# Optimization experiments

Hardware: AMD Instinct MI355X
Metric: run time of the kernel (lower is better)

Reference implementation:

```python
import jax, jax.numpy as jnp
import numpy as np

N_NODES = 100000
N_EDGES = 1600000
STATE_DIM = 128
HIDDEN_DIM = 128
ACTION_DIM = 16


def gcn_conv(x, edge_index, W, b, n_nodes):
    """PyG-style GCNConv: add self-loops, symmetric normalization, x@W then aggregate."""
    xw = x @ W  # [N, H]
    loops = jnp.arange(n_nodes, dtype=edge_index.dtype)
    src = jnp.concatenate([edge_index[0], loops])  # [E+N]
    dst = jnp.concatenate([edge_index[1], loops])
    ones = jnp.ones(src.shape[0], dtype=xw.dtype)
    deg = jax.ops.segment_sum(ones, dst, num_segments=n_nodes)  # degree of target nodes
    dinv = jnp.where(deg > 0, jax.lax.rsqrt(deg), 0.0)
    norm = dinv[src] * dinv[dst]  # [E+N]
    msg = xw[src] * norm[:, None]  # gather + scale (irregular access)
    out = jax.ops.segment_sum(msg, dst, num_segments=n_nodes)  # scatter-aggregate
    return out + b


def setup_inputs() -> dict:
    key = jax.random.key(0)
    ks = jax.random.split(key, 12)
    def lin(k, fan_in, shape):
        bound = 1.0 / np.sqrt(fan_in)
        return jax.random.uniform(k, shape, jnp.float32, -bound, bound)
    return {
        "x": jax.random.normal(ks[0], (N_NODES, STATE_DIM), jnp.float32),
        "edge_index": jax.random.randint(ks[1], (2, N_EDGES), 0, N_NODES, jnp.int64),
        "action": jax.random.normal(ks[2], (N_NODES, ACTION_DIM), jnp.float32),
        "gcn1_w": lin(ks[3], STATE_DIM, (STATE_DIM, HIDDEN_DIM)),
        "gcn1_b": lin(ks[4], STATE_DIM, (HIDDEN_DIM,)),
        "gcn2_w": lin(ks[5], HIDDEN_DIM, (HIDDEN_DIM, HIDDEN_DIM)),
        "gcn2_b": lin(ks[6], HIDDEN_DIM, (HIDDEN_DIM,)),
        "fc1_w": lin(ks[7], HIDDEN_DIM + ACTION_DIM, (HIDDEN_DIM + ACTION_DIM, HIDDEN_DIM)),
        "fc1_b": lin(ks[8], HIDDEN_DIM + ACTION_DIM, (HIDDEN_DIM,)),
        "fc2_w": lin(ks[9], HIDDEN_DIM, (HIDDEN_DIM, 1)),
        "fc2_b": lin(ks[10], HIDDEN_DIM, (1,)),
    }


def reference(x, edge_index, action, gcn1_w, gcn1_b, gcn2_w, gcn2_b, fc1_w, fc1_b, fc2_w, fc2_b):
    n = x.shape[0]
    h = jax.nn.relu(gcn_conv(x, edge_index, gcn1_w, gcn1_b, n))
    h = jax.nn.relu(gcn_conv(h, edge_index, gcn2_w, gcn2_b, n))
    h = jnp.concatenate([h, action], axis=-1)  # [N, H+A]
    h = jax.nn.relu(h @ fc1_w + fc1_b)
    q = h @ fc2_w + fc2_b  # [N, 1]
    return q.squeeze(-1)
```

## Files before the change

kernel.cpp:

```cpp
#include <hip/hip_runtime.h>
#include <hip/hip_bf16.h>

typedef unsigned short u16;
typedef unsigned int   u32;
typedef __attribute__((ext_vector_type(8))) short bf16x8;
typedef __attribute__((ext_vector_type(4))) float f32x4;

constexpr int NN = 100000;
constexpr int NE = 1600000;
constexpr int D  = 128;
constexpr size_t WS_NEED = 58909184;

constexpr int NBUCK = 196;
constexpr int NBLKA = 256;
constexpr int EPB   = 6272;
constexpr int CAPA  = 80;

__device__ __forceinline__ float bf2f(u16 u){ union{u32 i;float f;}v; v.i=((u32)u)<<16; return v.f; }
__device__ __forceinline__ float2 bfp(u32 u){ union{u32 i;float f;}a,b; a.i=u<<16; b.i=u&0xffff0000u; return make_float2(a.f,b.f); }
__device__ __forceinline__ u16 f2bf(float f){ union{float f;u32 i;}v; v.f=f; u32 r=v.i + 0x7fffu + ((v.i>>16)&1u); return (u16)(r>>16); }
__device__ __forceinline__ u32 pk2(float a, float b){ return (u32)f2bf(a) | ((u32)f2bf(b)<<16); }

__global__ void detect_kernel(const u32* __restrict__ xw, const int* __restrict__ ei,
                              int* __restrict__ flagf, int* __restrict__ flage){
  __shared__ int shf[256];
  __shared__ int she[256];
  int t = threadIdx.x;
  int cnt = 0;
  for(int i = 0; i < 16; i++){
    u32 w = xw[(t*16 + i) * 256];
    int e = (int)((w >> 7) & 0xFFu);
    cnt += (e >= 64 && e <= 160) ? 1 : 0;
  }
  int nz = 0;
  for(int i = 0; i < 8; i++){
    int k = t*8 + i;
    long long w = 1 + ((long long)k * (2LL*NE - 2)) / 2048;
    nz += (ei[(int)(w | 1)] != 0) ? 1 : 0;
  }
  shf[t] = cnt; she[t] = nz;
  __syncthreads();
  for(int off=128; off>0; off>>=1){
    if(t<off){ shf[t]+=shf[t+off]; she[t]+=she[t+off]; }
    __syncthreads();
  }
  if(t==0){ flagf[0] = (shf[0] < 3000) ? 1 : 0; flage[0] = (she[0] == 0) ? 1 : 0; }
}

__global__ void prep_kernel(const void* __restrict__ w1, const void* __restrict__ w2,
    const void* __restrict__ fw1, const void* __restrict__ b1, const void* __restrict__ b2,
    const void* __restrict__ fb1, const void* __restrict__ fw2, const void* __restrict__ fb2,
    const int* __restrict__ flagf,
    u16* __restrict__ WT1, u16* __restrict__ WT2, u16* __restrict__ WTF, float* __restrict__ BF)
{
  const int ff = flagf[0];
  int i = blockIdx.x*256 + threadIdx.x;
  auto cv = [&](const void* p, int idx)->float{
    return ff ? ((const float*)p)[idx] : bf2f(((const u16*)p)[idx]);
  };
  if(i < 16384){
    int k = i >> 7, d = i & 127;
    WT1[d*128 + k] = f2bf(cv(w1, i));
  }else if(i < 32768){
    int j = i - 16384; int k = j >> 7, d = j & 127;
    WT2[d*128 + k] = f2bf(cv(w2, j));
  }else if(i < 51200){
    int j = i - 32768; int k = j >> 7, d = j & 127;
    WTF[d*144 + k] = f2bf(cv(fw1, j));
  }else if(i < 51713){
    int j = i - 51200;
    if(j < 128)       BF[j]   = cv(b1, j);
    else if(j < 256)  BF[j]   = cv(b2, j-128);
    else if(j < 384)  BF[j]   = cv(fb1, j-256);
    else if(j < 512)  BF[j]   = cv(fw2, j-384);
    else              BF[512] = cv(fb2, 0);
  }
}

__global__ void fill1_kernel(u16* __restrict__ out, int n){
  int i = blockIdx.x*blockDim.x + threadIdx.x;
  if(i < n) out[i] = 0x3F80;
}

__global__ __launch_bounds__(256) void passA_kernel(
    const int* __restrict__ ei, const int* __restrict__ flage,
    u32* __restrict__ ebuf, u32* __restrict__ counts)
{
  __shared__ u32 hist[NBUCK];
  int t = threadIdx.x;
  for(int b = t; b < NBUCK; b += 256) hist[b] = 0;
  __syncthreads();
  const int f = flage[0];
  const int eb = blockIdx.x * EPB;
  const u32 cbase = blockIdx.x * NBUCK;
  for(int i = t; i < EPB; i += 256){
    int e = eb + i;
    if(e >= NE) break;
    int s = f ? ei[2*e]      : ei[e];
    int d = f ? ei[2*(NE+e)] : ei[NE+e];
    if((u32)s >= (u32)NN || (u32)d >= (u32)NN) continue;
    int b = d >> 9;
    u32 rank = atomicAdd(&hist[b], 1u);
    if(rank < CAPA) ebuf[(size_t)(cbase + b)*CAPA + rank] = (u32)s | ((u32)(d & 511) << 17);
  }
  __syncthreads();
  for(int b = t; b < NBUCK; b += 256){
    u32 c = hist[b];
    counts[cbase + b] = (c < CAPA) ? c : CAPA;
  }
}

__global__ void scan196_kernel(const u32* __restrict__ counts, int* __restrict__ bases){
  __shared__ int sh[NBUCK];
  int t = threadIdx.x;
  if(t < NBUCK){
    int tot = 0;
    for(int c = 0; c < NBLKA; c++) tot += counts[c*NBUCK + t];
    sh[t] = tot;
  }
  __syncthreads();
  if(t == 0){
    int acc = 0;
    for(int b = 0; b < NBUCK; b++){ int v = sh[b]; sh[b] = acc; acc += v; }
  }
  __syncthreads();
  if(t < NBUCK) bases[t] = sh[t];
}

__global__ __launch_bounds__(512) void passB_kernel(
    const u32* __restrict__ ebuf, const u32* __restrict__ counts, const int* __restrict__ bases,
    int* __restrict__ deg, int* __restrict__ off, float* __restrict__ dinv,
    int* __restrict__ srcs)
{
  __shared__ int cnt[512];
  __shared__ int nodeoff[512];
  __shared__ int pos[512];
  __shared__ int choff[NBLKA + 1];
  const int t = threadIdx.x;
  const int b = blockIdx.x;
  const int v0 = b << 9;

  cnt[t] = 0;
  __syncthreads();

  if(t < NBLKA) choff[t] = (int)counts[t*NBUCK + b];
  __syncthreads();
  if(t == 0){
    int acc = 0;
    for(int c = 0; c < NBLKA; c++){ int v = choff[c]; choff[c] = acc; acc += v; }
    choff[NBLKA] = acc;
  }
  __syncthreads();
  const int T = choff[NBLKA];

  for(int i = t; i < T; i += 512){
    int lo = 0, hi = NBLKA - 1;
    #pragma unroll
    for(int s = 0; s < 8; s++){
      int mid = (lo + hi) >> 1;
      if(choff[mid + 1] <= i) lo = mid + 1; else hi = mid;
    }
    u32 rec = ebuf[(size_t)(lo*NBUCK + b)*CAPA + (i - choff[lo])];
    atomicAdd(&cnt[rec >> 17], 1);
  }
  __syncthreads();

  int myc = cnt[t];
  nodeoff[t] = myc;
  __syncthreads();
  for(int o = 1; o < 512; o <<= 1){
    int a = (t >= o) ? nodeoff[t - o] : 0;
    __syncthreads();
    nodeoff[t] += a;
    __syncthreads();
  }
  int excl = nodeoff[t] - myc;
  __syncthreads();
  nodeoff[t] = excl;
  pos[t] = 0;
  __syncthreads();

  const int gb = bases[b];

  for(int i = t; i < T; i += 512){
    int lo = 0, hi = NBLKA - 1;
    #pragma unroll
    for(int s = 0; s < 8; s++){
      int mid = (lo + hi) >> 1;
      if(choff[mid + 1] <= i) lo = mid + 1; else hi = mid;
    }
    u32 rec = ebuf[(size_t)(lo*NBUCK + b)*CAPA + (i - choff[lo])];
    int ld = rec >> 17;
    int r = atomicAdd(&pos[ld], 1);
    srcs[gb + nodeoff[ld] + r] = (int)(rec & 0x1FFFFu);
  }

  int v = v0 + t;
  if(v < NN){
    deg[v] = myc;
    off[v] = gb + excl;
    dinv[v] = rsqrtf((float)(myc + 1));
  }
}

template<int K, bool FUSE_Q, bool RAW1, bool RAW2>
__global__ __launch_bounds__(256) void gemm_mfma(
    const void* __restrict__ A1, const void* __restrict__ A2,
    const u16* __restrict__ WT, const float* __restrict__ biasf,
    const float* __restrict__ qwf, const float* __restrict__ qbf,
    const int* __restrict__ flagf, void* __restrict__ out, int n)
{
  constexpr int KT = ((K + 31)/32)*32;
  constexpr int KP = KT + 8;
  __shared__ u16 Ws[128*KP];
  __shared__ u16 As[64*KP];
  const int tid = threadIdx.x;
  const int nb  = blockIdx.x * 64;
  const int ff  = flagf[0];

  constexpr int CPT = KT/8;
  for(int i = tid; i < 128*CPT; i += 256){
    int row = i / CPT, col = (i % CPT) * 8;
    uint4 v = make_uint4(0,0,0,0);
    if(col < K) v = *(const uint4*)(WT + row*K + col);
    *(uint4*)(Ws + row*KP + col) = v;
  }
  for(int i = tid; i < 64*CPT; i += 256){
    int row = i / CPT, col = (i % CPT) * 8;
    int gr = nb + row; if(gr >= n) gr = n-1;
    uint4 v = make_uint4(0,0,0,0);
    if(col < 128){
      if(!RAW1 || !ff){
        v = *(const uint4*)((const u16*)A1 + (size_t)gr*128 + col);
      }else{
        const float* af = (const float*)A1 + (size_t)gr*128 + col;
        float4 p0 = *(const float4*)(af);
        float4 p1 = *(const float4*)(af + 4);
        v.x = pk2(p0.x,p0.y); v.y = pk2(p0.z,p0.w);
        v.z = pk2(p1.x,p1.y); v.w = pk2(p1.z,p1.w);
      }
    }else if(col < K){
      if(!RAW2 || !ff){
        v = *(const uint4*)((const u16*)A2 + (size_t)gr*16 + (col - 128));
      }else{
        const float* af = (const float*)A2 + (size_t)gr*16 + (col - 128);
        float4 p0 = *(const float4*)(af);
        float4 p1 = *(const float4*)(af + 4);
        v.x = pk2(p0.x,p0.y); v.y = pk2(p0.z,p0.w);
        v.z = pk2(p1.x,p1.y); v.w = pk2(p1.z,p1.w);
      }
    }
    *(uint4*)(As + row*KP + col) = v;
  }
  __syncthreads();

  const int wave = tid >> 6;
  const int lane = tid & 63;
  const int quad = lane >> 4;
  const int lm   = lane & 15;

  const u16* Ab = As + (wave*16 + lm)*KP;
  const u16* Bb = Ws + lm*KP;

  f32x4 acc[8];
  #pragma unroll
  for(int t=0;t<8;t++) acc[t] = (f32x4){0.f,0.f,0.f,0.f};

  #pragma unroll
  for(int ki = 0; ki < KT/32; ki++){
    int kk = ki*32 + quad*8;
    bf16x8 a = *(const bf16x8*)(Ab + kk);
    #pragma unroll
    for(int t=0;t<8;t++){
      bf16x8 b = *(const bf16x8*)(Bb + t*16*KP + kk);
      acc[t] = __builtin_amdgcn_mfma_f32_16x16x32_bf16(a, b, acc[t], 0, 0, 0);
    }
  }

  const int node0 = nb + wave*16 + quad*4;
  if(!FUSE_Q){
    #pragma unroll
    for(int t=0;t<8;t++){
      #pragma unroll
      for(int r=0;r<4;r++){
        int gr = node0 + r;
        if(gr < n) ((u16*)out)[(size_t)gr*D + t*16 + lm] = f2bf(acc[t][r]);
      }
    }
  }else{
    float qp[4] = {0.f,0.f,0.f,0.f};
    #pragma unroll
    for(int t=0;t<8;t++){
      float bvt = biasf[t*16 + lm];
      float qwt = qwf[t*16 + lm];
      #pragma unroll
      for(int r=0;r<4;r++){
        float h = fmaxf(acc[t][r] + bvt, 0.f);
        qp[r] += h * qwt;
      }
    }
    #pragma unroll
    for(int r=0;r<4;r++){
      #pragma unroll
      for(int o=1; o<16; o<<=1) qp[r] += __shfl_xor(qp[r], o, 16);
    }
    if(lm == 0){
      float qb = qbf[0];
      #pragma unroll
      for(int r=0;r<4;r++){
        int gr = node0 + r;
        if(gr < n){
          float q = qp[r] + qb;
          if(ff) ((float*)out)[gr] = q;
          else   ((u16*)out)[gr]  = f2bf(q);
        }
      }
    }
  }
}

__global__ __launch_bounds__(256) void gather_kernel(
    const int* __restrict__ off, const int* __restrict__ deg,
    const int* __restrict__ srcs, const float* __restrict__ dinv,
    const u16* __restrict__ xw, const float* __restrict__ biasf,
    u16* __restrict__ h)
{
  int node = blockIdx.x*8 + (threadIdx.x >> 5);
  int lane = threadIdx.x & 31;
  if(node >= NN) return;
  int j0 = off[node];
  int j1 = j0 + deg[node];

  float a0=0.f, a1=0.f, a2=0.f, a3=0.f;
  const size_t lo = 4*lane;
  int j = j0;
  for(; j+4 <= j1; j += 4){
    int s0=srcs[j], s1=srcs[j+1], s2=srcs[j+2], s3=srcs[j+3];
    if((u32)s0>=(u32)NN) s0=node; if((u32)s1>=(u32)NN) s1=node;
    if((u32)s2>=(u32)NN) s2=node; if((u32)s3>=(u32)NN) s3=node;
    float w0=dinv[s0], w1=dinv[s1], w2=dinv[s2], w3=dinv[s3];
    uint2 p0 = *(const uint2*)(xw + (size_t)s0*D + lo);
    uint2 p1 = *(const uint2*)(xw + (size_t)s1*D + lo);
    uint2 p2 = *(const uint2*)(xw + (size_t)s2*D + lo);
    uint2 p3 = *(const uint2*)(xw + (size_t)s3*D + lo);
    float2 f0a=bfp(p0.x), f0b=bfp(p0.y);
    float2 f1a=bfp(p1.x), f1b=bfp(p1.y);
    float2 f2a=bfp(p2.x), f2b=bfp(p2.y);
    float2 f3a=bfp(p3.x), f3b=bfp(p3.y);
    a0 += w0*f0a.x + w1*f1a.x + w2*f2a.x + w3*f3a.x;
    a1 += w0*f0a.y + w1*f1a.y + w2*f2a.y + w3*f3a.y;
    a2 += w0*f0b.x + w1*f1b.x + w2*f2b.x + w3*f3b.x;
    a3 += w0*f0b.y + w1*f1b.y + w2*f2b.y + w3*f3b.y;
  }
  for(; j < j1; j++){
    int s = srcs[j];
    if((u32)s >= (u32)NN) continue;
    float w = dinv[s];
    uint2 p = *(const uint2*)(xw + (size_t)s*D + lo);
    float2 fa=bfp(p.x), fb=bfp(p.y);
    a0 += w*fa.x; a1 += w*fa.y; a2 += w*fb.x; a3 += w*fb.y;
  }

  float dv = dinv[node];
  float dv2 = dv*dv;
  uint2 ps = *(const uint2*)(xw + (size_t)node*D + lo);
  float2 sa=bfp(ps.x), sb=bfp(ps.y);
  float4 bf4 = *(const float4*)(biasf + lo);
  float o0 = fmaxf(dv*a0 + dv2*sa.x + bf4.x, 0.f);
  float o1 = fmaxf(dv*a1 + dv2*sa.y + bf4.y, 0.f);
  float o2 = fmaxf(dv*a2 + dv2*sb.x + bf4.z, 0.f);
  float o3 = fmaxf(dv*a3 + dv2*sb.y + bf4.w, 0.f);
  uint2 pkd; pkd.x = pk2(o0,o1); pkd.y = pk2(o2,o3);
  *(uint2*)(h + (size_t)node*D + lo) = pkd;
}

extern "C" void kernel_launch(void* const* d_in, const int* in_sizes, int n_in,
                              void* d_out, int out_size, void* d_ws, size_t ws_size,
                              hipStream_t stream)
{
  bool meta_ok = (n_in >= 11) && (in_sizes[0] == NN*D) && (in_sizes[1] == 2*NE)
              && (in_sizes[2] == NN*16) && (out_size == NN);
  if(!meta_ok){
    fill1_kernel<<<(NN+255)/256, 256, 0, stream>>>((u16*)d_out, NN);
    return;
  }
  if(ws_size < WS_NEED) return;

  const void* x      = d_in[0];
  const int*  ei     = (const int*)d_in[1];
  const void* action = d_in[2];
  const void* w1     = d_in[3];
  const void* b1     = d_in[4];
  const void* w2     = d_in[5];
  const void* b2     = d_in[6];
  const void* fw1    = d_in[7];
  const void* fb1    = d_in[8];
  const void* fw2    = d_in[9];
  const void* fb2    = d_in[10];

  char* ws = (char*)d_ws;
  int*   DEG    = (int*)(ws + 0);
  int*   OFF    = (int*)(ws + 400128);
  float* DINV   = (float*)(ws + 800256);
  int*   FLAGE  = (int*)(ws + 1204480);
  int*   FLAGF  = (int*)(ws + 1204544);
  u16*   WT1    = (u16*)(ws + 1204608);
  u16*   WT2    = (u16*)(ws + 1237376);
  u16*   WTF    = (u16*)(ws + 1270144);
  float* BF     = (float*)(ws + 1307008);
  int*   SRCS   = (int*)(ws + 1309184);
  u16*   F0     = (u16*)(ws + 7709184);
  u16*   F1     = (u16*)(ws + 33309184);
  u32*   EBUF   = (u32*)(ws + 33309184);
  u32*   COUNTS = (u32*)(ws + 49365504);
  int*   BASES  = (int*)(ws + 49566208);

  detect_kernel<<<1, 256, 0, stream>>>((const u32*)x, ei, FLAGF, FLAGE);

  passA_kernel<<<NBLKA, 256, 0, stream>>>(ei, FLAGE, EBUF, COUNTS);
  scan196_kernel<<<1, 256, 0, stream>>>(COUNTS, BASES);
  passB_kernel<<<NBUCK, 512, 0, stream>>>(EBUF, COUNTS, BASES, DEG, OFF, DINV, SRCS);

  prep_kernel<<<203, 256, 0, stream>>>(w1, w2, fw1, b1, b2, fb1, fw2, fb2, FLAGF,
                                       WT1, WT2, WTF, BF);

  gemm_mfma<128,false,true,false><<<(NN+63)/64, 256, 0, stream>>>(x, nullptr, WT1, nullptr, nullptr, nullptr, FLAGF, F0, NN);
  gather_kernel<<<(NN+7)/8, 256, 0, stream>>>(OFF, DEG, SRCS, DINV, F0, BF, F1);

  gemm_mfma<128,false,false,false><<<(NN+63)/64, 256, 0, stream>>>(F1, nullptr, WT2, nullptr, nullptr, nullptr, FLAGF, F0, NN);
  gather_kernel<<<(NN+7)/8, 256, 0, stream>>>(OFF, DEG, SRCS, DINV, F0, BF+128, F1);

  gemm_mfma<144,true,false,true><<<(NN+63)/64, 256, 0, stream>>>(F1, action, WTF, BF+256, BF+384, BF+512, FLAGF, d_out, NN);
}
```

Before: 372.0 us.

## Pre-scale GEMM output by dinv and widen gather to 16 lanes per node

The GEMM epilogue now multiplies each output row by its source node's dinv, so the gather kernel no longer loads dinv per edge and only applies the destination scale at the end, with the self-loop folded into the sum. The gather kernel now uses 16 lanes per node with 16-byte loads, 16 nodes per block, and software-prefetches the next four source indices with nontemporal loads. This removes per-edge dinv gathers and bounds checks and halves the load instruction count. The trade-off is that the invalid-index guard and the node<NN check are dropped, and the pre-scale adds one extra bf16 rounding of the scaled features.

Measured after the change: 364.2 us. -2.1%, faster.

```diff
diff --git a/kernel.cpp b/kernel.cpp
--- a/kernel.cpp
+++ b/kernel.cpp
@@ -208,7 +208,8 @@
     const void* __restrict__ A1, const void* __restrict__ A2,
     const u16* __restrict__ WT, const float* __restrict__ biasf,
     const float* __restrict__ qwf, const float* __restrict__ qbf,
-    const int* __restrict__ flagf, void* __restrict__ out, int n)
+    const int* __restrict__ flagf, const float* __restrict__ dscale,
+    void* __restrict__ out, int n)
 {
   constexpr int KT = ((K + 31)/32)*32;
   constexpr int KP = KT + 8;
@@ -280,11 +281,14 @@
   const int node0 = nb + wave*16 + quad*4;
   if(!FUSE_Q){
     #pragma unroll
-    for(int t=0;t<8;t++){
-      #pragma unroll
-      for(int r=0;r<4;r++){
-        int gr = node0 + r;
-        if(gr < n) ((u16*)out)[(size_t)gr*D + t*16 + lm] = f2bf(acc[t][r]);
+    for(int r=0;r<4;r++){
+      int gr = node0 + r;
+      if(gr < n){
+        float dv = dscale[gr];
+        #pragma unroll
+        for(int t=0;t<8;t++){
+          ((u16*)out)[(size_t)gr*D + t*16 + lm] = f2bf(acc[t][r]*dv);
+        }
       }
     }
   }else{
@@ -319,59 +323,76 @@
   }
 }
 
+#define ACC8(r)  { float2 f_;                       \
+    f_ = bfp((r).x); a0 += f_.x; a1 += f_.y;        \
+    f_ = bfp((r).y); a2 += f_.x; a3 += f_.y;        \
+    f_ = bfp((r).z); a4 += f_.x; a5 += f_.y;        \
+    f_ = bfp((r).w); a6 += f_.x; a7 += f_.y; }
+
 __global__ __launch_bounds__(256) void gather_kernel(
     const int* __restrict__ off, const int* __restrict__ deg,
     const int* __restrict__ srcs, const float* __restrict__ dinv,
     const u16* __restrict__ xw, const float* __restrict__ biasf,
     u16* __restrict__ h)
 {
-  int node = blockIdx.x*8 + (threadIdx.x >> 5);
-  int lane = threadIdx.x & 31;
-  if(node >= NN) return;
-  int j0 = off[node];
-  int j1 = j0 + deg[node];
-
-  float a0=0.f, a1=0.f, a2=0.f, a3=0.f;
-  const size_t lo = 4*lane;
+  const int node = blockIdx.x*16 + (threadIdx.x >> 4);
+  const int lane = threadIdx.x & 15;
+  const int j0 = off[node];
+  const int j1 = j0 + deg[node];
+
+  float a0=0.f,a1=0.f,a2=0.f,a3=0.f,a4=0.f,a5=0.f,a6=0.f,a7=0.f;
+  const u16* __restrict__ xl = xw + 8*lane;
+
   int j = j0;
-  for(; j+4 <= j1; j += 4){
-    int s0=srcs[j], s1=srcs[j+1], s2=srcs[j+2], s3=srcs[j+3];
-    if((u32)s0>=(u32)NN) s0=node; if((u32)s1>=(u32)NN) s1=node;
-    if((u32)s2>=(u32)NN) s2=node; if((u32)s3>=(u32)NN) s3=node;
-    float w0=dinv[s0], w1=dinv[s1], w2=dinv[s2], w3=dinv[s3];
-    uint2 p0 = *(const uint2*)(xw + (size_t)s0*D + lo);
-    uint2 p1 = *(const uint2*)(xw + (size_t)s1*D + lo);
-    uint2 p2 = *(const uint2*)(xw + (size_t)s2*D + lo);
-    uint2 p3 = *(const uint2*)(xw + (size_t)s3*D + lo);
-    float2 f0a=bfp(p0.x), f0b=bfp(p0.y);
-    float2 f1a=bfp(p1.x), f1b=bfp(p1.y);
-    float2 f2a=bfp(p2.x), f2b=bfp(p2.y);
-    float2 f3a=bfp(p3.x), f3b=bfp(p3.y);
-    a0 += w0*f0a.x + w1*f1a.x + w2*f2a.x + w3*f3a.x;
-    a1 += w0*f0a.y + w1*f1a.y + w2*f2a.y + w3*f3a.y;
-    a2 += w0*f0b.x + w1*f1b.x + w2*f2b.x + w3*f3b.x;
-    a3 += w0*f0b.y + w1*f1b.y + w2*f2b.y + w3*f3b.y;
+  int s0=0, s1=0, s2=0, s3=0;
+  const bool pre = (j + 4 <= j1);
+  if(pre){
+    s0 = __builtin_nontemporal_load(&srcs[j]);
+    s1 = __builtin_nontemporal_load(&srcs[j+1]);
+    s2 = __builtin_nontemporal_load(&srcs[j+2]);
+    s3 = __builtin_nontemporal_load(&srcs[j+3]);
+  }
+  for(; j + 8 <= j1; j += 4){
+    uint4 r0 = *(const uint4*)(xl + (size_t)s0*D);
+    uint4 r1 = *(const uint4*)(xl + (size_t)s1*D);
+    uint4 r2 = *(const uint4*)(xl + (size_t)s2*D);
+    uint4 r3 = *(const uint4*)(xl + (size_t)s3*D);
+    s0 = __builtin_nontemporal_load(&srcs[j+4]);
+    s1 = __builtin_nontemporal_load(&srcs[j+5]);
+    s2 = __builtin_nontemporal_load(&srcs[j+6]);
+    s3 = __builtin_nontemporal_load(&srcs[j+7]);
+    ACC8(r0); ACC8(r1); ACC8(r2); ACC8(r3);
+  }
+  if(pre){
+    uint4 r0 = *(const uint4*)(xl + (size_t)s0*D);
+    uint4 r1 = *(const uint4*)(xl + (size_t)s1*D);
+    uint4 r2 = *(const uint4*)(xl + (size_t)s2*D);
+    uint4 r3 = *(const uint4*)(xl + (size_t)s3*D);
+    ACC8(r0); ACC8(r1); ACC8(r2); ACC8(r3);
+    j += 4;
   }
   for(; j < j1; j++){
-    int s = srcs[j];
-    if((u32)s >= (u32)NN) continue;
-    float w = dinv[s];
-    uint2 p = *(const uint2*)(xw + (size_t)s*D + lo);
-    float2 fa=bfp(p.x), fb=bfp(p.y);
-    a0 += w*fa.x; a1 += w*fa.y; a2 += w*fb.x; a3 += w*fb.y;
-  }
-
-  float dv = dinv[node];
-  float dv2 = dv*dv;
-  uint2 ps = *(const uint2*)(xw + (size_t)node*D + lo);
-  float2 sa=bfp(ps.x), sb=bfp(ps.y);
-  float4 bf4 = *(const float4*)(biasf + lo);
-  float o0 = fmaxf(dv*a0 + dv2*sa.x + bf4.x, 0.f);
-  float o1 = fmaxf(dv*a1 + dv2*sa.y + bf4.y, 0.f);
-  float o2 = fmaxf(dv*a2 + dv2*sb.x + bf4.z, 0.f);
-  float o3 = fmaxf(dv*a3 + dv2*sb.y + bf4.w, 0.f);
-  uint2 pkd; pkd.x = pk2(o0,o1); pkd.y = pk2(o2,o3);
-  *(uint2*)(h + (size_t)node*D + lo) = pkd;
+    int s = __builtin_nontemporal_load(&srcs[j]);
+    uint4 r = *(const uint4*)(xl + (size_t)s*D);
+    ACC8(r);
+  }
+
+  uint4 ps = *(const uint4*)(xl + (size_t)node*D);
+  ACC8(ps);
+  const float dv = dinv[node];
+  float4 bA = *(const float4*)(biasf + 8*lane);
+  float4 bB = *(const float4*)(biasf + 8*lane + 4);
+  float o0 = fmaxf(fmaf(dv,a0,bA.x), 0.f);
+  float o1 = fmaxf(fmaf(dv,a1,bA.y), 0.f);
+  float o2 = fmaxf(fmaf(dv,a2,bA.z), 0.f);
+  float o3 = fmaxf(fmaf(dv,a3,bA.w), 0.f);
+  float o4 = fmaxf(fmaf(dv,a4,bB.x), 0.f);
+  float o5 = fmaxf(fmaf(dv,a5,bB.y), 0.f);
+  float o6 = fmaxf(fmaf(dv,a6,bB.z), 0.f);
+  float o7 = fmaxf(fmaf(dv,a7,bB.w), 0.f);
+  uint4 pkd;
+  pkd.x = pk2(o0,o1); pkd.y = pk2(o2,o3); pkd.z = pk2(o4,o5); pkd.w = pk2(o6,o7);
+  *(uint4*)(h + (size_t)node*D + 8*lane) = pkd;
 }
 
 extern "C" void kernel_launch(void* const* d_in, const int* in_sizes, int n_in,
@@ -424,11 +445,11 @@
   prep_kernel<<<203, 256, 0, stream>>>(w1, w2, fw1, b1, b2, fb1, fw2, fb2, FLAGF,
                                        WT1, WT2, WTF, BF);
 
-  gemm_mfma<128,false,true,false><<<(NN+63)/64, 256, 0, stream>>>(x, nullptr, WT1, nullptr, nullptr, nullptr, FLAGF, F0, NN);
-  gather_kernel<<<(NN+7)/8, 256, 0, stream>>>(OFF, DEG, SRCS, DINV, F0, BF, F1);
-
-  gemm_mfma<128,false,false,false><<<(NN+63)/64, 256, 0, stream>>>(F1, nullptr, WT2, nullptr, nullptr, nullptr, FLAGF, F0, NN);
-  gather_kernel<<<(NN+7)/8, 256, 0, stream>>>(OFF, DEG, SRCS, DINV, F0, BF+128, F1);
-
-  gemm_mfma<144,true,false,true><<<(NN+63)/64, 256, 0, stream>>>(F1, action, WTF, BF+256, BF+384, BF+512, FLAGF, d_out, NN);
-}
+  gemm_mfma<128,false,true,false><<<(NN+63)/64, 256, 0, stream>>>(x, nullptr, WT1, nullptr, nullptr, nullptr, FLAGF, DINV, F0, NN);
+  gather_kernel<<<(NN+15)/16, 256, 0, stream>>>(OFF, DEG, SRCS, DINV, F0, BF, F1);
+
+  gemm_mfma<128,false,false,false><<<(NN+63)/64, 256, 0, stream>>>(F1, nullptr, WT2, nullptr, nullptr, nullptr, FLAGF, DINV, F0, NN);
+  gather_kernel<<<(NN+15)/16, 256, 0, stream>>>(OFF, DEG, SRCS, DINV, F0, BF+128, F1);
+
+  gemm_mfma<144,true,false,true><<<(NN+63)/64, 256, 0, stream>>>(F1, action, WTF, BF+256, BF+384, BF+512, FLAGF, nullptr, d_out, NN);
+}
```
